# Kernel tuning notes

Hardware: AMD Instinct MI355X
Metric: run time of the kernel (lower is better)

The kernel has to match this reference:

```python
import jax, jax.numpy as jnp
import numpy as np

NUM_LABELS = 32
EMB = 128          # label_embedding_dim
HID = 1024         # hidden_dim (== encoder feature dim)
B, S = 128, 512


def setup_inputs() -> dict:
    key = jax.random.key(0)
    ks = jax.random.split(key, 8)
    k = 1.0 / np.sqrt(HID)  # torch GRU/Linear default init bound
    u = lambda kk, shape: jax.random.uniform(kk, shape, jnp.float32, minval=-k, maxval=k)
    return {
        "hidden_states": jax.random.normal(ks[0], (B, S, HID), jnp.float32),
        "emb": jax.random.normal(ks[1], (NUM_LABELS, EMB), jnp.float32),  # nn.Embedding ~ N(0,1)
        "W_ih": u(ks[2], (3 * HID, EMB + HID)),  # GRU input weights, gate order r,z,n
        "W_hh": u(ks[3], (3 * HID, HID)),
        "b_ih": u(ks[4], (3 * HID,)),
        "b_hh": u(ks[5], (3 * HID,)),
        "W_out": u(ks[6], (NUM_LABELS, HID)),
        "b_out": u(ks[7], (NUM_LABELS,)),
    }


def reference(hidden_states, emb, W_ih, W_hh, b_ih, b_hh, W_out, b_out):
    batch = hidden_states.shape[0]
    h0 = jnp.zeros((batch, W_hh.shape[1]), hidden_states.dtype)
    lab0 = jnp.broadcast_to(emb[0], (batch, emb.shape[1]))  # label_start_embedding (id 0)

    def step(carry, x_t):
        h, lab = carry
        inp = jnp.concatenate([x_t, lab], axis=-1)            # [B, HID+EMB]
        gi = inp @ W_ih.T + b_ih                               # [B, 3*HID]
        gh = h @ W_hh.T + b_hh
        ir, iz, in_ = jnp.split(gi, 3, axis=-1)
        hr, hz, hn = jnp.split(gh, 3, axis=-1)
        r = jax.nn.sigmoid(ir + hr)
        z = jax.nn.sigmoid(iz + hz)
        n = jnp.tanh(in_ + r * hn)
        h_new = (1.0 - z) * n + z * h                          # PyTorch GRU update
        logit = h_new @ W_out.T + b_out                        # dropout is identity in eval
        pred = jnp.argmax(logit, axis=-1)                      # softmax is monotone; argmax(probs)==argmax(logit)
        return (h_new, emb[pred]), logit

    xs = jnp.swapaxes(hidden_states, 0, 1)                     # [S, B, HID]
    _, logits = jax.lax.scan(step, (h0, lab0), xs)             # logits: [S, B, L]
    return jnp.swapaxes(logits, 0, 1)                          # [B, S, L]
```

## Files before the change

### kernel.cpp

```cpp
#include <hip/hip_runtime.h>


#define S_    512
#define HID_  1024
#define EMB_  128
#define NL_   32
#define G3_   3072

#define LDS_A_STRIDE 1032
#define LDS_A_BYTES  (48 * LDS_A_STRIDE * 2)
#define CP_STRIDE    52
#define LDS_CP_BYTES (4 * 64 * CP_STRIDE * 4)
#define LDS_BYTES    (LDS_A_BYTES + LDS_CP_BYTES)

typedef __attribute__((ext_vector_type(8))) short          short8;
typedef __attribute__((ext_vector_type(8))) unsigned short u16x8;
typedef __attribute__((ext_vector_type(4))) unsigned short u16x4;
typedef __attribute__((ext_vector_type(4))) float          f32x4;
typedef unsigned long long u64_t;

__device__ unsigned int   g_ctr[576];
__device__ unsigned int   g_flag[1];
__device__ unsigned int   g_vis[256];
__device__ unsigned int   g_hseq[2][64 * 16];
__device__ unsigned int   g_predw[128 * 16];
__device__ unsigned short g_hhi[2][128 * HID_];
__device__ unsigned short g_hlo[2][128 * HID_];
__device__ float          g_hf32[2][128 * HID_];
__device__ float          g_Glab[NL_ * G3_];
__device__ unsigned short g_Wlox[G3_ * HID_];
__device__ unsigned short g_Wlohh[G3_ * HID_];
__device__ float          g_GIXall[(size_t)S_ * 128 * 64 * 48];

__device__ __forceinline__ float bf2f(unsigned short u) {
  union { unsigned int i; float f; } v; v.i = ((unsigned int)u) << 16; return v.f;
}
__device__ __forceinline__ unsigned short f2bf(float f) {
  union { float f; unsigned int i; } v; v.f = f;
  unsigned int u = v.i;
  return (unsigned short)((u + 0x7FFFu + ((u >> 16) & 1u)) >> 16);
}
__device__ __forceinline__ short8 ld_bf8(const unsigned short* p) {
  return __builtin_bit_cast(short8, *(const u16x8*)p);
}
__device__ __forceinline__ float ldin(const void* p, long i, int f32) {
  return f32 ? ((const float*)p)[i] : bf2f(((const unsigned short*)p)[i]);
}
__device__ __forceinline__ void store_out(void* out, int f32, long idx, float v) {
  if (f32) ((float*)out)[idx] = v;
  else     ((unsigned short*)out)[idx] = f2bf(v);
}

__device__ __forceinline__ u64_t ald64(const void* p) {
  return __hip_atomic_load((const u64_t*)p, __ATOMIC_RELAXED,
                           __HIP_MEMORY_SCOPE_AGENT);
}
__device__ __forceinline__ unsigned int ald32(const unsigned int* p) {
  return __hip_atomic_load(p, __ATOMIC_RELAXED, __HIP_MEMORY_SCOPE_AGENT);
}
__device__ __forceinline__ void ast32(unsigned int* p, unsigned int v) {
  __hip_atomic_store(p, v, __ATOMIC_RELAXED, __HIP_MEMORY_SCOPE_AGENT);
}

__global__ void k_zero() {
  int t = blockIdx.x * 256 + threadIdx.x;
  if (t < 576) g_ctr[t] = 0u;
  else if (t < 832) g_vis[t - 576] = 0u;
  if (t >= 2048 && t < 4096) ((unsigned int*)g_hseq)[t - 2048] = 0u;
  if (t >= 4096 && t < 6144) g_predw[t - 4096] = 0u;
  const u16x4 z4 = {0, 0, 0, 0};
  const f32x4 zf = {0.f, 0.f, 0.f, 0.f};
  for (int i = t; i < 2 * 128 * HID_ / 4; i += 65536) {
    ((u16x4*)g_hhi)[i] = z4;
    ((u16x4*)g_hlo)[i] = z4;
    ((f32x4*)g_hf32)[i] = zf;
  }
}

__global__ void k_detect(const unsigned short* __restrict__ W) {
  unsigned bad = 0;
  for (int i = threadIdx.x; i < 1024; i += 64) {
    float v = bf2f(W[i]);
    if (!(v * v <= 1.0f)) bad = 1;
  }
  unsigned long long b = __ballot(bad != 0);
  if (threadIdx.x == 0) g_flag[0] = (b != 0ull) ? 1u : 0u;
}

__global__ void k_prep(const void* __restrict__ emb,
                       const void* __restrict__ W_ih,
                       const void* __restrict__ b_ih) {
  const int f32 = (int)g_flag[0];
  int l = blockIdx.x / 12;
  int n = (blockIdx.x % 12) * 256 + threadIdx.x;
  double acc = (double)ldin(b_ih, n, f32);
  for (int e = 0; e < EMB_; ++e)
    acc += (double)ldin(emb, (long)l * EMB_ + e, f32) *
           (double)ldin(W_ih, (long)n * (HID_ + EMB_) + HID_ + e, f32);
  g_Glab[l * G3_ + n] = (float)acc;
}

__global__ void k_prepw(const void* __restrict__ W_ih,
                        const void* __restrict__ W_hh) {
  if (!g_flag[0]) return;
  long i4 = ((long)blockIdx.x * 256 + threadIdx.x) * 4;
  if (i4 >= (long)G3_ * HID_) return;
  int row = (int)(i4 >> 10), col = (int)(i4 & 1023);
  f32x4 wh = *(const f32x4*)&((const float*)W_hh)[(long)row * HID_ + col];
  f32x4 wx = *(const f32x4*)&((const float*)W_ih)[(long)row * (HID_ + EMB_) + col];
  u16x4 lh, lx;
  #pragma unroll
  for (int j = 0; j < 4; ++j) {
    unsigned short h1 = f2bf(wh[j]);
    lh[j] = f2bf(wh[j] - bf2f(h1));
    unsigned short x1 = f2bf(wx[j]);
    lx[j] = f2bf(wx[j] - bf2f(x1));
  }
  *(u16x4*)&g_Wlohh[i4] = lh;
  *(u16x4*)&g_Wlox[i4]  = lx;
}

__device__ __forceinline__ void gridbar(int wg, int bar) {
  __syncthreads();
  if (threadIdx.x == 0) {
    asm volatile("s_waitcnt vmcnt(0)" ::: "memory");
    unsigned int* c1   = g_ctr + (wg & 7) * 64;
    unsigned int* root = g_ctr + 512;
    unsigned int old = __hip_atomic_fetch_add(c1, 1u, __ATOMIC_RELAXED,
                                              __HIP_MEMORY_SCOPE_AGENT);
    if (old == 32u * (unsigned)(bar + 1) - 1u)
      __hip_atomic_fetch_add(root, 1u, __ATOMIC_RELAXED,
                             __HIP_MEMORY_SCOPE_AGENT);
    unsigned int tgt = 8u * (unsigned)(bar + 1);
    while (__hip_atomic_load(root, __ATOMIC_RELAXED,
                             __HIP_MEMORY_SCOPE_AGENT) < tgt)
      __builtin_amdgcn_s_sleep(1);
  }
  __syncthreads();
}

__device__ __forceinline__ void wait_hseq_acq(int half, int it) {
  if (threadIdx.x < 64) {
    const unsigned int* p = &g_hseq[half][threadIdx.x * 16];
    while ((int)ald32(p) < it) { }
  }
  __builtin_amdgcn_sched_barrier(0);
  __syncthreads();
  if (threadIdx.x == 0)
    __builtin_amdgcn_fence(__ATOMIC_ACQUIRE, "agent");
  __syncthreads();
}

__device__ __forceinline__ void stage_w(unsigned short* sA, const void* Wsrc,
                                        int wstride, int rg, int f32, int tid) {
  if (f32) {
    const float* Ws = (const float*)Wsrc;
    for (int i = tid; i < 48 * 1024 / 4; i += 256) {
      int e = i * 4, row = e >> 10, k4 = e & 1023;
      int grow = (row >> 4) * HID_ + rg * 16 + (row & 15);
      f32x4 v = *(const f32x4*)&Ws[(long)grow * wstride + k4];
      u16x4 o;
      #pragma unroll
      for (int j = 0; j < 4; ++j) o[j] = f2bf(v[j]);
      *(u16x4*)&sA[row * LDS_A_STRIDE + k4] = o;
    }
  } else {
    const unsigned short* Ws = (const unsigned short*)Wsrc;
    for (int i = tid; i < 48 * 1024 / 4; i += 256) {
      int e = i * 4, row = e >> 10, k4 = e & 1023;
      int grow = (row >> 4) * HID_ + rg * 16 + (row & 15);
      *(u16x4*)&sA[row * LDS_A_STRIDE + k4] =
          *(const u16x4*)&Ws[(long)grow * wstride + k4];
    }
  }
}

__global__ __launch_bounds__(256) void k_seq(
    const void* __restrict__ hs,
    const void* __restrict__ W_ih,
    const void* __restrict__ W_hh,
    const void* __restrict__ b_hh,
    const void* __restrict__ W_out,
    const void* __restrict__ b_out,
    void* __restrict__ out) {
  extern __shared__ char smem[];
  unsigned short* sA  = (unsigned short*)smem;
  float*          sCp = (float*)(smem + LDS_A_BYTES);

  const int f32 = (int)g_flag[0];
  const int tid = threadIdx.x;
  const int wg  = blockIdx.x;
  const bool isx = (wg < 128);
  const int lid  = isx ? wg : wg - 128;
  const int rg = lid >> 1, bg = lid & 1;
  const int slot = lid;
  const int lane = tid & 63, wv = tid >> 6;
  const int m = lane & 15, q = lane >> 4;
  const int bl = tid & 63;
  const int jj = (tid >> 6) * 4;
  const int kw0 = wv * 256 + q * 8;

  int bar = 0;

  if (tid == 0) ast32(&g_vis[wg], (unsigned)wg + 1u);
  gridbar(wg, bar); ++bar;
  if (tid == 0) {
    unsigned p = ((unsigned)wg + 37u) & 255u;
    if (ald32(&g_vis[p]) != p + 1u) store_out(out, f32, wg, 999.0f);
  }

  {
    const int slot0 = wg & 127;
    const int rg0 = slot0 >> 1, bg0 = slot0 & 1;
    stage_w(sA, W_ih, HID_ + EMB_, rg0, f32, tid);
    __syncthreads();
    const long bstride = (long)S_ * HID_;
    const long boffb = (long)(bg0 * 64) * S_ * HID_;
    for (int t = 0; t < 256; ++t) {
      const int it = ((wg >> 7) << 8) | t;
      f32x4 acc[3][4];
      #pragma unroll
      for (int rt = 0; rt < 3; ++rt)
        #pragma unroll
        for (int bt = 0; bt < 4; ++bt) acc[rt][bt] = f32x4{0.f, 0.f, 0.f, 0.f};
      const long boff = boffb + (long)it * HID_;
      if (f32) {
        const float* Bf = (const float*)hs + boff;
        #pragma unroll
        for (int kb = 0; kb < 8; ++kb) {
          const int k = kw0 + kb * 32;
          short8 avh[3];
          #pragma unroll
          for (int rt = 0; rt < 3; ++rt)
            avh[rt] = ld_bf8(&sA[(rt * 16 + m) * LDS_A_STRIDE + k]);
          short8 bxh[4], bxl[4];
          #pragma unroll
          for (int bt = 0; bt < 4; ++bt) {
            const float* bp = Bf + (long)(bt * 16 + m) * bstride + k;
            f32x4 x0 = *(const f32x4*)bp;
            f32x4 x1 = *(const f32x4*)(bp + 4);
            u16x8 th, tl;
            #pragma unroll
            for (int j = 0; j < 4; ++j) {
              unsigned short u0 = f2bf(x0[j]);
              th[j] = u0; tl[j] = f2bf(x0[j] - bf2f(u0));
              unsigned short u1 = f2bf(x1[j]);
              th[4 + j] = u1; tl[4 + j] = f2bf(x1[j] - bf2f(u1));
            }
            bxh[bt] = __builtin_bit_cast(short8, th);
            bxl[bt] = __builtin_bit_cast(short8, tl);
          }
          short8 avl[3];
          #pragma unroll
          for (int rt = 0; rt < 3; ++rt)
            avl[rt] = ld_bf8(&g_Wlox[(long)(rt * HID_ + rg0 * 16 + m) * HID_ + k]);
          #pragma unroll
          for (int rt = 0; rt < 3; ++rt)
            #pragma unroll
            for (int bt = 0; bt < 4; ++bt) {
              acc[rt][bt] = __builtin_amdgcn_mfma_f32_16x16x32_bf16(
                  avh[rt], bxh[bt], acc[rt][bt], 0, 0, 0);
              acc[rt][bt] = __builtin_amdgcn_mfma_f32_16x16x32_bf16(
                  avh[rt], bxl[bt], acc[rt][bt], 0, 0, 0);
              acc[rt][bt] = __builtin_amdgcn_mfma_f32_16x16x32_bf16(
                  avl[rt], bxh[bt], acc[rt][bt], 0, 0, 0);
              acc[rt][bt] = __builtin_amdgcn_mfma_f32_16x16x32_bf16(
                  avl[rt], bxl[bt], acc[rt][bt], 0, 0, 0);
            }
        }
      } else {
        const unsigned short* Bh = (const unsigned short*)hs + boff;
        #pragma unroll
        for (int kb = 0; kb < 8; ++kb) {
          const int k = kw0 + kb * 32;
          short8 avh[3], bxh[4];
          #pragma unroll
          for (int rt = 0; rt < 3; ++rt)
            avh[rt] = ld_bf8(&sA[(rt * 16 + m) * LDS_A_STRIDE + k]);
          #pragma unroll
          for (int bt = 0; bt < 4; ++bt)
            bxh[bt] = ld_bf8(&Bh[(long)(bt * 16 + m) * bstride + k]);
          #pragma unroll
          for (int rt = 0; rt < 3; ++rt)
            #pragma unroll
            for (int bt = 0; bt < 4; ++bt)
              acc[rt][bt] = __builtin_amdgcn_mfma_f32_16x16x32_bf16(
                  avh[rt], bxh[bt], acc[rt][bt], 0, 0, 0);
        }
      }
      __syncthreads();
      #pragma unroll
      for (int rt = 0; rt < 3; ++rt)
        #pragma unroll
        for (int bt = 0; bt < 4; ++bt)
          *(f32x4*)&sCp[(wv * 64 + bt * 16 + m) * CP_STRIDE + rt * 16 + q * 4] =
              acc[rt][bt];
      __syncthreads();
      #pragma unroll
      for (int g = 0; g < 3; ++g) {
        f32x4 sv = f32x4{0.f, 0.f, 0.f, 0.f};
        #pragma unroll
        for (int w = 0; w < 4; ++w)
          sv += *(const f32x4*)&sCp[(w * 64 + bl) * CP_STRIDE + g * 16 + jj];
        *(f32x4*)&g_GIXall[(((long)it * 128 + slot0) * 64 + bl) * 48 +
                           g * 16 + jj] = sv;
      }
      __syncthreads();
    }
  }
  __threadfence();
  gridbar(wg, bar); ++bar;

  if (!isx) stage_w(sA, W_hh, HID_, rg, f32, tid);
  __syncthreads();

  float bo = 0.f;
  if (isx && tid < 32) bo = ldin(b_out, tid, f32);
  f32x4 bhh[3];
  if (!isx) {
    const int jbase = rg * 16 + jj;
    #pragma unroll
    for (int g = 0; g < 3; ++g)
      #pragma unroll
      for (int t = 0; t < 4; ++t)
        bhh[g][t] = ldin(b_hh, (long)g * HID_ + jbase + t, f32);
  }

  float hreg[4] = {0.f, 0.f, 0.f, 0.f};
  f32x4 sred[3];

  for (int it = 0; it <= S_; ++it) {
    if (isx && it >= 1) {
      wait_hseq_acq(wg >> 6, it);
      const int rb = (it + 1) & 1;
      if (it == 1 && wg == 0 && tid == 0) {
        float s = 0.f;
        for (int i = 0; i < 32; ++i) s += g_hf32[0][i] * g_hf32[0][i];
        if (s == 0.f) store_out(out, f32, 300, 555.0f);
      }
      const int b = wg, s = it - 1;
      float* scrp  = sCp;
      float* shrow = sCp + 256;
      {
        f32x4 hv = *(const f32x4*)&g_hf32[rb][(long)b * HID_ + tid * 4];
        *(f32x4*)&shrow[(tid >> 5) * 132 + (tid & 31) * 4] = hv;
      }
      __syncthreads();
      {
        int l = tid >> 3, kc = tid & 7;
        const float* hr = shrow + kc * 132;
        float p = 0.f;
        if (f32) {
          const float* wr = (const float*)W_out + (long)l * HID_ + kc * 128;
          for (int k = 0; k < 128; k += 4) {
            f32x4 wa = *(const f32x4*)&wr[k];
            f32x4 ha = *(const f32x4*)&hr[k];
            #pragma unroll
            for (int j = 0; j < 4; ++j) p += wa[j] * ha[j];
          }
        } else {
          const unsigned short* wr =
              (const unsigned short*)W_out + (long)l * HID_ + kc * 128;
          for (int k = 0; k < 128; k += 8) {
            u16x8 w8 = *(const u16x8*)&wr[k];
            f32x4 ha = *(const f32x4*)&hr[k];
            f32x4 hb = *(const f32x4*)&hr[k + 4];
            #pragma unroll
            for (int j = 0; j < 4; ++j) {
              p += bf2f(w8[j]) * ha[j];
              p += bf2f(w8[4 + j]) * hb[j];
            }
          }
        }
        scrp[tid] = p;
      }
      __syncthreads();
      if (tid < 32) {
        const float* pp = sCp + tid * 8;
        float v = pp[0] + pp[1] + pp[2] + pp[3] + pp[4] + pp[5] + pp[6] + pp[7]
                  + bo;
        store_out(out, f32, ((long)b * S_ + s) * NL_ + tid, v);
        float bv = v; int bi = tid;
        #pragma unroll
        for (int off = 16; off; off >>= 1) {
          float v2 = __shfl_down(bv, off, 32);
          int   i2 = __shfl_down(bi, off, 32);
          if (v2 > bv || (v2 == bv && i2 < bi)) { bv = v2; bi = i2; }
        }
        if (tid == 0) ast32(&g_predw[b * 16], ((unsigned)it << 8) | (unsigned)bi);
      }
      __syncthreads();
    }

    if (!isx && it < S_) {
      f32x4 gixp[3];
      #pragma unroll
      for (int g = 0; g < 3; ++g)
        gixp[g] = *(const f32x4*)&g_GIXall[(((long)it * 128 + slot) * 64 + bl)
                                           * 48 + g * 16 + jj];

      wait_hseq_acq(bg, it);
      const int rb = (it + 1) & 1;
      const int wb = it & 1;

      f32x4 acc[3][4];
      #pragma unroll
      for (int rt = 0; rt < 3; ++rt)
        #pragma unroll
        for (int bt = 0; bt < 4; ++bt) acc[rt][bt] = f32x4{0.f, 0.f, 0.f, 0.f};

      const unsigned short* Bhi = g_hhi[rb] + (long)(bg * 64) * HID_;
      const unsigned short* Blo = g_hlo[rb] + (long)(bg * 64) * HID_;
      #pragma unroll
      for (int kb = 0; kb < 8; ++kb) {
        const int k = kw0 + kb * 32;
        short8 avh[3], bh[4], blv[4];
        #pragma unroll
        for (int rt = 0; rt < 3; ++rt)
          avh[rt] = ld_bf8(&sA[(rt * 16 + m) * LDS_A_STRIDE + k]);
        #pragma unroll
        for (int bt = 0; bt < 4; ++bt) {
          bh[bt]  = ld_bf8(&Bhi[(long)(bt * 16 + m) * HID_ + k]);
          blv[bt] = ld_bf8(&Blo[(long)(bt * 16 + m) * HID_ + k]);
        }
        #pragma unroll
        for (int rt = 0; rt < 3; ++rt)
          #pragma unroll
          for (int bt = 0; bt < 4; ++bt) {
            acc[rt][bt] = __builtin_amdgcn_mfma_f32_16x16x32_bf16(
                avh[rt], bh[bt], acc[rt][bt], 0, 0, 0);
            acc[rt][bt] = __builtin_amdgcn_mfma_f32_16x16x32_bf16(
                avh[rt], blv[bt], acc[rt][bt], 0, 0, 0);
          }
        if (f32) {
          short8 avl[3];
          #pragma unroll
          for (int rt = 0; rt < 3; ++rt)
            avl[rt] = ld_bf8(&g_Wlohh[(long)(rt * HID_ + rg * 16 + m) * HID_ + k]);
          #pragma unroll
          for (int rt = 0; rt < 3; ++rt)
            #pragma unroll
            for (int bt = 0; bt < 4; ++bt) {
              acc[rt][bt] = __builtin_amdgcn_mfma_f32_16x16x32_bf16(
                  avl[rt], bh[bt], acc[rt][bt], 0, 0, 0);
              acc[rt][bt] = __builtin_amdgcn_mfma_f32_16x16x32_bf16(
                  avl[rt], blv[bt], acc[rt][bt], 0, 0, 0);
            }
        }
      }

      __syncthreads();
      #pragma unroll
      for (int rt = 0; rt < 3; ++rt)
        #pragma unroll
        for (int bt = 0; bt < 4; ++bt)
          *(f32x4*)&sCp[(wv * 64 + bt * 16 + m) * CP_STRIDE + rt * 16 + q * 4] =
              acc[rt][bt];
      __syncthreads();
      #pragma unroll
      for (int g = 0; g < 3; ++g) {
        f32x4 sv = f32x4{0.f, 0.f, 0.f, 0.f};
        #pragma unroll
        for (int w = 0; w < 4; ++w)
          sv += *(const f32x4*)&sCp[(w * 64 + bl) * CP_STRIDE + g * 16 + jj];
        sred[g] = sv;
      }

      const int bglob = bg * 64 + bl;
      int pb = 0;
      if (it >= 1) {
        const unsigned int* pw = &g_predw[bglob * 16];
        unsigned w = ald32(pw);
        while ((int)(w >> 8) < it) { w = ald32(pw); }
        pb = (int)(w & 255u);
      }
      __builtin_amdgcn_sched_barrier(0);

      const int jbase = rg * 16 + jj;
      const float* gl = g_Glab + (long)pb * G3_;
      f32x4 glab[3];
      #pragma unroll
      for (int g = 0; g < 3; ++g)
        glab[g] = *(const f32x4*)&gl[g * HID_ + jbase];
      u16x4 whi, wlo;
      f32x4 hf;
      #pragma unroll
      for (int t4 = 0; t4 < 4; ++t4) {
        float ghr = sred[0][t4] + bhh[0][t4];
        float ghz = sred[1][t4] + bhh[1][t4];
        float ghn = sred[2][t4] + bhh[2][t4];
        float gir = gixp[0][t4] + glab[0][t4];
        float giz = gixp[1][t4] + glab[1][t4];
        float gin = gixp[2][t4] + glab[2][t4];
        float r = 1.f / (1.f + expf(-(gir + ghr)));
        float z = 1.f / (1.f + expf(-(giz + ghz)));
        float n = tanhf(gin + r * ghn);
        float hn = (1.f - z) * n + z * hreg[t4];
        hreg[t4] = hn;
        hf[t4] = hn;
        unsigned short uhi = f2bf(hn);
        whi[t4] = uhi;
        wlo[t4] = f2bf(hn - bf2f(uhi));
      }
      *(u16x4*)&g_hhi[wb][(long)bglob * HID_ + jbase] = whi;
      *(u16x4*)&g_hlo[wb][(long)bglob * HID_ + jbase] = wlo;
      *(f32x4*)&g_hf32[wb][(long)bglob * HID_ + jbase] = hf;

      asm volatile("s_waitcnt vmcnt(0)" ::: "memory");
      __syncthreads();
      if (tid == 0) {
        __builtin_amdgcn_fence(__ATOMIC_RELEASE, "agent");
        ast32(&g_hseq[bg][rg * 16], (unsigned)(it + 1));
      }
    }
  }
}

extern "C" void kernel_launch(void* const* d_in, const int* in_sizes, int n_in,
                              void* d_out, int out_size, void* d_ws, size_t ws_size,
                              hipStream_t stream) {
  const void* hs    = d_in[0];
  const void* emb   = d_in[1];
  const void* W_ih  = d_in[2];
  const void* W_hh  = d_in[3];
  const void* b_ih  = d_in[4];
  const void* b_hh  = d_in[5];
  const void* W_out = d_in[6];
  const void* b_out = d_in[7];

  hipLaunchKernelGGL(k_zero, dim3(256), dim3(256), 0, stream);
  hipLaunchKernelGGL(k_detect, dim3(1), dim3(64), 0, stream,
                     (const unsigned short*)W_ih);
  hipLaunchKernelGGL(k_prep, dim3(32 * 12), dim3(256), 0, stream,
                     emb, W_ih, b_ih);
  hipLaunchKernelGGL(k_prepw, dim3(3072), dim3(256), 0, stream, W_ih, W_hh);
  hipFuncSetAttribute((const void*)k_seq,
                      hipFuncAttributeMaxDynamicSharedMemorySize, LDS_BYTES);
  hipLaunchKernelGGL(k_seq, dim3(256), dim3(256), LDS_BYTES, stream,
                     hs, W_ih, W_hh, b_hh, W_out, b_out, d_out);
}
```

Measured before the change: 15.23 ms.

## Split input-projection precompute into separate kernel and hoist label wait

Moves the input-projection GEMM (W_ih times hidden states for all timesteps) out of the persistent recurrent kernel into its own launch, replacing one grid barrier with a kernel boundary. The wait on the previous step's predicted label and the gather of its embedding contribution are moved before the LDS partial-sum reduction, so they overlap with it. Spin loops gain s_sleep, which cuts memory polling traffic at the cost of slightly higher wake-up latency. The extra launch adds fixed overhead, and the split relies on the launch boundary to make the precomputed GIX values visible.

After: 15.20 ms. No clear change (-0.2%).

```diff
diff --git a/kernel.cpp b/kernel.cpp
--- a/kernel.cpp
+++ b/kernel.cpp
@@ -51,10 +51,6 @@
   else     ((unsigned short*)out)[idx] = f2bf(v);
 }
 
-__device__ __forceinline__ u64_t ald64(const void* p) {
-  return __hip_atomic_load((const u64_t*)p, __ATOMIC_RELAXED,
-                           __HIP_MEMORY_SCOPE_AGENT);
-}
 __device__ __forceinline__ unsigned int ald32(const unsigned int* p) {
   return __hip_atomic_load(p, __ATOMIC_RELAXED, __HIP_MEMORY_SCOPE_AGENT);
 }
@@ -134,7 +130,7 @@
     unsigned int tgt = 8u * (unsigned)(bar + 1);
     while (__hip_atomic_load(root, __ATOMIC_RELAXED,
                              __HIP_MEMORY_SCOPE_AGENT) < tgt)
-      __builtin_amdgcn_s_sleep(1);
+      __builtin_amdgcn_s_sleep(2);
   }
   __syncthreads();
 }
@@ -142,7 +138,7 @@
 __device__ __forceinline__ void wait_hseq_acq(int half, int it) {
   if (threadIdx.x < 64) {
     const unsigned int* p = &g_hseq[half][threadIdx.x * 16];
-    while ((int)ald32(p) < it) { }
+    while ((int)ald32(p) < it) __builtin_amdgcn_s_sleep(1);
   }
   __builtin_amdgcn_sched_barrier(0);
   __syncthreads();
@@ -175,9 +171,121 @@
   }
 }
 
-__global__ __launch_bounds__(256) void k_seq(
-    const void* __restrict__ hs,
-    const void* __restrict__ W_ih,
+__global__ __launch_bounds__(256) void k_gix(const void* __restrict__ hs,
+                                             const void* __restrict__ W_ih) {
+  extern __shared__ char smem[];
+  unsigned short* sA  = (unsigned short*)smem;
+  float*          sCp = (float*)(smem + LDS_A_BYTES);
+
+  const int f32 = (int)g_flag[0];
+  const int tid = threadIdx.x;
+  const int wg  = blockIdx.x;
+  const int lane = tid & 63, wv = tid >> 6;
+  const int m = lane & 15, q = lane >> 4;
+  const int bl = tid & 63;
+  const int jj = (tid >> 6) * 4;
+  const int kw0 = wv * 256 + q * 8;
+
+  const int slot0 = wg & 127;
+  const int rg0 = slot0 >> 1, bg0 = slot0 & 1;
+  stage_w(sA, W_ih, HID_ + EMB_, rg0, f32, tid);
+  __syncthreads();
+  const long bstride = (long)S_ * HID_;
+  const long boffb = (long)(bg0 * 64) * S_ * HID_;
+  for (int t = 0; t < 256; ++t) {
+    const int it = ((wg >> 7) << 8) | t;
+    f32x4 acc[3][4];
+    #pragma unroll
+    for (int rt = 0; rt < 3; ++rt)
+      #pragma unroll
+      for (int bt = 0; bt < 4; ++bt) acc[rt][bt] = f32x4{0.f, 0.f, 0.f, 0.f};
+    const long boff = boffb + (long)it * HID_;
+    if (f32) {
+      const float* Bf = (const float*)hs + boff;
+      #pragma unroll
+      for (int kb = 0; kb < 8; ++kb) {
+        const int k = kw0 + kb * 32;
+        short8 avh[3];
+        #pragma unroll
+        for (int rt = 0; rt < 3; ++rt)
+          avh[rt] = ld_bf8(&sA[(rt * 16 + m) * LDS_A_STRIDE + k]);
+        short8 bxh[4], bxl[4];
+        #pragma unroll
+        for (int bt = 0; bt < 4; ++bt) {
+          const float* bp = Bf + (long)(bt * 16 + m) * bstride + k;
+          f32x4 x0 = *(const f32x4*)bp;
+          f32x4 x1 = *(const f32x4*)(bp + 4);
+          u16x8 th, tl;
+          #pragma unroll
+          for (int j = 0; j < 4; ++j) {
+            unsigned short u0 = f2bf(x0[j]);
+            th[j] = u0; tl[j] = f2bf(x0[j] - bf2f(u0));
+            unsigned short u1 = f2bf(x1[j]);
+            th[4 + j] = u1; tl[4 + j] = f2bf(x1[j] - bf2f(u1));
+          }
+          bxh[bt] = __builtin_bit_cast(short8, th);
+          bxl[bt] = __builtin_bit_cast(short8, tl);
+        }
+        short8 avl[3];
+        #pragma unroll
+        for (int rt = 0; rt < 3; ++rt)
+          avl[rt] = ld_bf8(&g_Wlox[(long)(rt * HID_ + rg0 * 16 + m) * HID_ + k]);
+        #pragma unroll
+        for (int rt = 0; rt < 3; ++rt)
+          #pragma unroll
+          for (int bt = 0; bt < 4; ++bt) {
+            acc[rt][bt] = __builtin_amdgcn_mfma_f32_16x16x32_bf16(
+                avh[rt], bxh[bt], acc[rt][bt], 0, 0, 0);
+            acc[rt][bt] = __builtin_amdgcn_mfma_f32_16x16x32_bf16(
+                avh[rt], bxl[bt], acc[rt][bt], 0, 0, 0);
+            acc[rt][bt] = __builtin_amdgcn_mfma_f32_16x16x32_bf16(
+                avl[rt], bxh[bt], acc[rt][bt], 0, 0, 0);
+            acc[rt][bt] = __builtin_amdgcn_mfma_f32_16x16x32_bf16(
+                avl[rt], bxl[bt], acc[rt][bt], 0, 0, 0);
+          }
+      }
+    } else {
+      const unsigned short* Bh = (const unsigned short*)hs + boff;
+      #pragma unroll
+      for (int kb = 0; kb < 8; ++kb) {
+        const int k = kw0 + kb * 32;
+        short8 avh[3], bxh[4];
+        #pragma unroll
+        for (int rt = 0; rt < 3; ++rt)
+          avh[rt] = ld_bf8(&sA[(rt * 16 + m) * LDS_A_STRIDE + k]);
+        #pragma unroll
+        for (int bt = 0; bt < 4; ++bt)
+          bxh[bt] = ld_bf8(&Bh[(long)(bt * 16 + m) * bstride + k]);
+        #pragma unroll
+        for (int rt = 0; rt < 3; ++rt)
+          #pragma unroll
+          for (int bt = 0; bt < 4; ++bt)
+            acc[rt][bt] = __builtin_amdgcn_mfma_f32_16x16x32_bf16(
+                avh[rt], bxh[bt], acc[rt][bt], 0, 0, 0);
+      }
+    }
+    __syncthreads();
+    #pragma unroll
+    for (int rt = 0; rt < 3; ++rt)
+      #pragma unroll
+      for (int bt = 0; bt < 4; ++bt)
+        *(f32x4*)&sCp[(wv * 64 + bt * 16 + m) * CP_STRIDE + rt * 16 + q * 4] =
+            acc[rt][bt];
+    __syncthreads();
+    #pragma unroll
+    for (int g = 0; g < 3; ++g) {
+      f32x4 sv = f32x4{0.f, 0.f, 0.f, 0.f};
+      #pragma unroll
+      for (int w = 0; w < 4; ++w)
+        sv += *(const f32x4*)&sCp[(w * 64 + bl) * CP_STRIDE + g * 16 + jj];
+      *(f32x4*)&g_GIXall[(((long)it * 128 + slot0) * 64 + bl) * 48 +
+                         g * 16 + jj] = sv;
+    }
+    __syncthreads();
+  }
+}
+
+__global__ __launch_bounds__(256) void k_loop(
     const void* __restrict__ W_hh,
     const void* __restrict__ b_hh,
     const void* __restrict__ W_out,
@@ -200,116 +308,12 @@
   const int jj = (tid >> 6) * 4;
   const int kw0 = wv * 256 + q * 8;
 
-  int bar = 0;
-
   if (tid == 0) ast32(&g_vis[wg], (unsigned)wg + 1u);
-  gridbar(wg, bar); ++bar;
+  gridbar(wg, 0);
   if (tid == 0) {
     unsigned p = ((unsigned)wg + 37u) & 255u;
     if (ald32(&g_vis[p]) != p + 1u) store_out(out, f32, wg, 999.0f);
   }
-
-  {
-    const int slot0 = wg & 127;
-    const int rg0 = slot0 >> 1, bg0 = slot0 & 1;
-    stage_w(sA, W_ih, HID_ + EMB_, rg0, f32, tid);
-    __syncthreads();
-    const long bstride = (long)S_ * HID_;
-    const long boffb = (long)(bg0 * 64) * S_ * HID_;
-    for (int t = 0; t < 256; ++t) {
-      const int it = ((wg >> 7) << 8) | t;
-      f32x4 acc[3][4];
-      #pragma unroll
-      for (int rt = 0; rt < 3; ++rt)
-        #pragma unroll
-        for (int bt = 0; bt < 4; ++bt) acc[rt][bt] = f32x4{0.f, 0.f, 0.f, 0.f};
-      const long boff = boffb + (long)it * HID_;
-      if (f32) {
-        const float* Bf = (const float*)hs + boff;
-        #pragma unroll
-        for (int kb = 0; kb < 8; ++kb) {
-          const int k = kw0 + kb * 32;
-          short8 avh[3];
-          #pragma unroll
-          for (int rt = 0; rt < 3; ++rt)
-            avh[rt] = ld_bf8(&sA[(rt * 16 + m) * LDS_A_STRIDE + k]);
-          short8 bxh[4], bxl[4];
-          #pragma unroll
-          for (int bt = 0; bt < 4; ++bt) {
-            const float* bp = Bf + (long)(bt * 16 + m) * bstride + k;
-            f32x4 x0 = *(const f32x4*)bp;
-            f32x4 x1 = *(const f32x4*)(bp + 4);
-            u16x8 th, tl;
-            #pragma unroll
-            for (int j = 0; j < 4; ++j) {
-              unsigned short u0 = f2bf(x0[j]);
-              th[j] = u0; tl[j] = f2bf(x0[j] - bf2f(u0));
-              unsigned short u1 = f2bf(x1[j]);
-              th[4 + j] = u1; tl[4 + j] = f2bf(x1[j] - bf2f(u1));
-            }
-            bxh[bt] = __builtin_bit_cast(short8, th);
-            bxl[bt] = __builtin_bit_cast(short8, tl);
-          }
-          short8 avl[3];
-          #pragma unroll
-          for (int rt = 0; rt < 3; ++rt)
-            avl[rt] = ld_bf8(&g_Wlox[(long)(rt * HID_ + rg0 * 16 + m) * HID_ + k]);
-          #pragma unroll
-          for (int rt = 0; rt < 3; ++rt)
-            #pragma unroll
-            for (int bt = 0; bt < 4; ++bt) {
-              acc[rt][bt] = __builtin_amdgcn_mfma_f32_16x16x32_bf16(
-                  avh[rt], bxh[bt], acc[rt][bt], 0, 0, 0);
-              acc[rt][bt] = __builtin_amdgcn_mfma_f32_16x16x32_bf16(
-                  avh[rt], bxl[bt], acc[rt][bt], 0, 0, 0);
-              acc[rt][bt] = __builtin_amdgcn_mfma_f32_16x16x32_bf16(
-                  avl[rt], bxh[bt], acc[rt][bt], 0, 0, 0);
-              acc[rt][bt] = __builtin_amdgcn_mfma_f32_16x16x32_bf16(
-                  avl[rt], bxl[bt], acc[rt][bt], 0, 0, 0);
-            }
-        }
-      } else {
-        const unsigned short* Bh = (const unsigned short*)hs + boff;
-        #pragma unroll
-        for (int kb = 0; kb < 8; ++kb) {
-          const int k = kw0 + kb * 32;
-          short8 avh[3], bxh[4];
-          #pragma unroll
-          for (int rt = 0; rt < 3; ++rt)
-            avh[rt] = ld_bf8(&sA[(rt * 16 + m) * LDS_A_STRIDE + k]);
-          #pragma unroll
-          for (int bt = 0; bt < 4; ++bt)
-            bxh[bt] = ld_bf8(&Bh[(long)(bt * 16 + m) * bstride + k]);
-          #pragma unroll
-          for (int rt = 0; rt < 3; ++rt)
-            #pragma unroll
-            for (int bt = 0; bt < 4; ++bt)
-              acc[rt][bt] = __builtin_amdgcn_mfma_f32_16x16x32_bf16(
-                  avh[rt], bxh[bt], acc[rt][bt], 0, 0, 0);
-        }
-      }
-      __syncthreads();
-      #pragma unroll
-      for (int rt = 0; rt < 3; ++rt)
-        #pragma unroll
-        for (int bt = 0; bt < 4; ++bt)
-          *(f32x4*)&sCp[(wv * 64 + bt * 16 + m) * CP_STRIDE + rt * 16 + q * 4] =
-              acc[rt][bt];
-      __syncthreads();
-      #pragma unroll
-      for (int g = 0; g < 3; ++g) {
-        f32x4 sv = f32x4{0.f, 0.f, 0.f, 0.f};
-        #pragma unroll
-        for (int w = 0; w < 4; ++w)
-          sv += *(const f32x4*)&sCp[(w * 64 + bl) * CP_STRIDE + g * 16 + jj];
-        *(f32x4*)&g_GIXall[(((long)it * 128 + slot0) * 64 + bl) * 48 +
-                           g * 16 + jj] = sv;
-      }
-      __syncthreads();
-    }
-  }
-  __threadfence();
-  gridbar(wg, bar); ++bar;
 
   if (!isx) stage_w(sA, W_hh, HID_, rg, f32, tid);
   __syncthreads();
@@ -449,6 +453,24 @@
         }
       }
 
+      const int bglob = bg * 64 + bl;
+      const int jbase = rg * 16 + jj;
+      int pb = 0;
+      if (it >= 1) {
+        const unsigned int* pw = &g_predw[bglob * 16];
+        unsigned w = ald32(pw);
+        while ((int)(w >> 8) < it) {
+          __builtin_amdgcn_s_sleep(1);
+          w = ald32(pw);
+        }
+        pb = (int)(w & 255u);
+      }
+      const float* gl = g_Glab + (long)pb * G3_;
+      f32x4 glab[3];
+      #pragma unroll
+      for (int g = 0; g < 3; ++g)
+        glab[g] = *(const f32x4*)&gl[g * HID_ + jbase];
+
       __syncthreads();
       #pragma unroll
       for (int rt = 0; rt < 3; ++rt)
@@ -466,22 +488,6 @@
         sred[g] = sv;
       }
 
-      const int bglob = bg * 64 + bl;
-      int pb = 0;
-      if (it >= 1) {
-        const unsigned int* pw = &g_predw[bglob * 16];
-        unsigned w = ald32(pw);
-        while ((int)(w >> 8) < it) { w = ald32(pw); }
-        pb = (int)(w & 255u);
-      }
-      __builtin_amdgcn_sched_barrier(0);
-
-      const int jbase = rg * 16 + jj;
-      const float* gl = g_Glab + (long)pb * G3_;
-      f32x4 glab[3];
-      #pragma unroll
-      for (int g = 0; g < 3; ++g)
-        glab[g] = *(const f32x4*)&gl[g * HID_ + jbase];
       u16x4 whi, wlo;
       f32x4 hf;
       #pragma unroll
@@ -534,8 +540,11 @@
   hipLaunchKernelGGL(k_prep, dim3(32 * 12), dim3(256), 0, stream,
                      emb, W_ih, b_ih);
   hipLaunchKernelGGL(k_prepw, dim3(3072), dim3(256), 0, stream, W_ih, W_hh);
-  hipFuncSetAttribute((const void*)k_seq,
+  hipFuncSetAttribute((const void*)k_gix,
                       hipFuncAttributeMaxDynamicSharedMemorySize, LDS_BYTES);
-  hipLaunchKernelGGL(k_seq, dim3(256), dim3(256), LDS_BYTES, stream,
-                     hs, W_ih, W_hh, b_hh, W_out, b_out, d_out);
-}
+  hipFuncSetAttribute((const void*)k_loop,
+                      hipFuncAttributeMaxDynamicSharedMemorySize, LDS_BYTES);
+  hipLaunchKernelGGL(k_gix, dim3(256), dim3(256), LDS_BYTES, stream, hs, W_ih);
+  hipLaunchKernelGGL(k_loop, dim3(256), dim3(256), LDS_BYTES, stream,
+                     W_hh, b_hh, W_out, b_out, d_out);
+}
```
